# Optimization experiments

Hardware: AMD Instinct MI355X
Metric: run time of the kernel (lower is better)

The kernel has to match this reference:

```python
import jax, jax.numpy as jnp
import numpy as np

B, S, V, D, H, L, C = 64, 128, 50000, 300, 128, 20, 3
EPS = 1e-8


def lstm(x, w_ih, w_hh, b):
    # x: (B,S,D) -> outputs (B,S,H); torch gate order i,f,g,o
    xg = jnp.einsum('bsd,gd->bsg', x, w_ih) + b  # (B,S,4H)
    Hh = w_hh.shape[1]

    def step(carry, xt):
        hprev, cprev = carry
        g = xt + hprev @ w_hh.T
        i, f, gg, o = jnp.split(g, 4, axis=-1)
        c = jax.nn.sigmoid(f) * cprev + jax.nn.sigmoid(i) * jnp.tanh(gg)
        hnew = jax.nn.sigmoid(o) * jnp.tanh(c)
        return (hnew, c), hnew

    z = jnp.zeros((x.shape[0], Hh), x.dtype)
    _, hs = jax.lax.scan(step, (z, z), xg.transpose(1, 0, 2))
    return hs.transpose(1, 0, 2)


def bilstm(x, wih_f, whh_f, b_f, wih_b, whh_b, b_b):
    fwd = lstm(x, wih_f, whh_f, b_f)
    bwd = jnp.flip(lstm(jnp.flip(x, 1), wih_b, whh_b, b_b), 1)
    return jnp.concatenate([fwd, bwd], axis=-1)


def safe_div(prod, norm):
    # matches module's cosine_similarity eps handling
    return prod / jnp.where(norm > EPS, norm, EPS)


def full_matching(p1, p2, w):
    # p1: (B,S,H), p2: (B,H), w: (H,L) -> (B,S,L)
    v1 = p1[:, :, :, None] * w          # (B,S,H,L)
    v2 = p2[:, :, None] * w             # (B,H,L)
    dot = jnp.einsum('bshl,bhl->bsl', v1, v2)
    n1 = jnp.linalg.norm(v1, axis=2)    # (B,S,L)
    n2 = jnp.linalg.norm(v2, axis=1)    # (B,L)
    return dot / (jnp.maximum(n1, EPS) * jnp.maximum(n2, EPS)[:, None, :])


def maxpool_matching(p1, p2, w):
    v1 = p1[..., None] * w              # (B,S,H,L)
    v2 = p2[..., None] * w              # (B,T,H,L)
    prod = jnp.einsum('bshl,bthl->blst', v1, v2)
    n1 = jnp.linalg.norm(v1, axis=2)    # (B,S,L)
    n2 = jnp.linalg.norm(v2, axis=2)    # (B,T,L)
    deno = jnp.einsum('bsl,btl->blst', n1, n2)
    return safe_div(prod, deno).max(axis=3).transpose(0, 2, 1)  # (B,S,L)


def _wcos(a, b, w):
    # F.cosine_similarity over hidden dim of a*w vs b*w -> (B,S,L)
    va = a[..., None] * w
    vb = b[..., None] * w
    dot = jnp.einsum('bshl,bshl->bsl', va, vb)
    na = jnp.linalg.norm(va, axis=2)
    nb = jnp.linalg.norm(vb, axis=2)
    return dot / (jnp.maximum(na, EPS) * jnp.maximum(nb, EPS))


def attentive_matching(p1, p2, w_att, w_max):
    n1 = jnp.linalg.norm(p1, axis=2, keepdims=True)   # (B,S,1)
    n2 = jnp.linalg.norm(p2, axis=2, keepdims=True)   # (B,T,1)
    alpha = safe_div(jnp.einsum('bsh,bth->bst', p1, p2),
                     n1 * n2.transpose(0, 2, 1))       # (B,S,T)
    max_idx = jnp.argmax(alpha, axis=2)                # (B,S)
    h_mat = jnp.einsum('bst,bth->bsh', alpha, p2)
    resultant = h_mat / alpha.sum(axis=2, keepdims=True)
    result_match = _wcos(resultant, p1, w_att)
    out_mat = jnp.take_along_axis(p2, max_idx[..., None], axis=1)  # (B,S,H)
    result_max = _wcos(out_mat, p1, w_max)
    return result_match, result_max


def setup_inputs() -> dict:
    key = jax.random.key(0)
    ks = jax.random.split(key, 32)
    g = lambda k, shp, s=0.05: (jax.random.normal(k, shp, jnp.float32) * s)
    inp = {
        'emb': g(ks[0], (V, D), 0.1),
        'ctx_wih_f': g(ks[1], (4 * H, D)), 'ctx_whh_f': g(ks[2], (4 * H, H)), 'ctx_b_f': jnp.zeros((4 * H,), jnp.float32),
        'ctx_wih_b': g(ks[3], (4 * H, D)), 'ctx_whh_b': g(ks[4], (4 * H, H)), 'ctx_b_b': jnp.zeros((4 * H,), jnp.float32),
        'agg_wih_f': g(ks[5], (4 * H, 8 * L)), 'agg_whh_f': g(ks[6], (4 * H, H)), 'agg_b_f': jnp.zeros((4 * H,), jnp.float32),
        'agg_wih_b': g(ks[7], (4 * H, 8 * L)), 'agg_whh_b': g(ks[8], (4 * H, H)), 'agg_b_b': jnp.zeros((4 * H,), jnp.float32),
        'pW1': g(ks[9], (2 * H, 4 * H)), 'pb1': jnp.zeros((2 * H,), jnp.float32),
        'pW2': g(ks[10], (C, 2 * H)), 'pb2': jnp.zeros((C,), jnp.float32),
        'p': jax.random.randint(ks[11], (B, S), 0, V),
        'h': jax.random.randint(ks[12], (B, S), 0, V),
    }
    for i in range(1, 9):
        inp[f'w{i}'] = g(ks[12 + i], (H, L), 0.5)
    return inp


def reference(emb, ctx_wih_f, ctx_whh_f, ctx_b_f, ctx_wih_b, ctx_whh_b, ctx_b_b,
              agg_wih_f, agg_whh_f, agg_b_f, agg_wih_b, agg_whh_b, agg_b_b,
              pW1, pb1, pW2, pb2, w1, w2, w3, w4, w5, w6, w7, w8, p, h):
    p1_in = emb[p]
    p2_in = emb[h]
    c1 = bilstm(p1_in, ctx_wih_f, ctx_whh_f, ctx_b_f, ctx_wih_b, ctx_whh_b, ctx_b_b)
    c2 = bilstm(p2_in, ctx_wih_f, ctx_whh_f, ctx_b_f, ctx_wih_b, ctx_whh_b, ctx_b_b)
    c1f, c1b = jnp.split(c1, 2, axis=-1)
    c2f, c2b = jnp.split(c2, 2, axis=-1)

    match_p1_f = full_matching(c1f, c2f[:, -1], w1)
    match_p1_b = full_matching(c1b, c2b[:, -1], w2)
    match_p2_f = full_matching(c2f, c1f[:, -1], w1)
    match_p2_b = full_matching(c2b, c1b[:, -1], w2)

    maxm_p1_f = maxpool_matching(c1f, c2f, w3)
    maxm_p1_b = maxpool_matching(c1b, c2b, w4)
    maxm_p2_f = maxpool_matching(c2f, c1f, w3)
    maxm_p2_b = maxpool_matching(c2b, c1b, w4)

    att_p1_f, attm_p1_f = attentive_matching(c1f, c2f, w5, w7)
    att_p1_b, attm_p1_b = attentive_matching(c1b, c2b, w6, w8)
    att_p2_f, attm_p2_f = attentive_matching(c2f, c1f, w5, w7)
    att_p2_b, attm_p2_b = attentive_matching(c2b, c1b, w6, w8)

    aggr_p1 = jnp.concatenate([match_p1_f, match_p1_b, maxm_p1_f, maxm_p1_b,
                               att_p1_f, att_p1_b, attm_p1_f, attm_p1_b], axis=2)
    aggr_p2 = jnp.concatenate([match_p2_f, match_p2_b, maxm_p2_f, maxm_p2_b,
                               att_p2_f, att_p2_b, attm_p2_f, attm_p2_b], axis=2)

    agg_p = bilstm(aggr_p1, agg_wih_f, agg_whh_f, agg_b_f, agg_wih_b, agg_whh_b, agg_b_b)
    agg_h = bilstm(aggr_p2, agg_wih_f, agg_whh_f, agg_b_f, agg_wih_b, agg_whh_b, agg_b_b)
    out = jnp.concatenate([agg_p[:, -1], agg_h[:, -1]], axis=1)  # (B,4H)
    out = jax.nn.relu(out @ pW1.T + pb1) @ pW2.T + pb2
    return out
```

## Files before the change

kernel.cpp:

```cpp
#include <hip/hip_runtime.h>
#include <math.h>

#define B_  64
#define S_  128
#define H_  128
#define D_  300
#define L_  20
#define G4  512
#define SH  (S_*H_)
#define BSH ((size_t)B_*SH)
#define EPSV 1e-8f

typedef __attribute__((ext_vector_type(8))) short bshort8;
typedef __attribute__((ext_vector_type(4))) float f32x4;

__device__ __forceinline__ unsigned fmap(float f){
  unsigned u = __float_as_uint(f);
  return (u & 0x80000000u) ? ~u : (u | 0x80000000u);
}
__device__ __forceinline__ float funmap(unsigned u){
  return __uint_as_float((u & 0x80000000u) ? (u & 0x7fffffffu) : ~u);
}
__device__ __forceinline__ float sigmf(float x){ return 1.f/(1.f+expf(-x)); }
__device__ __forceinline__ float dot4(float4 a, float4 b){
  return a.x*b.x + a.y*b.y + a.z*b.z + a.w*b.w;
}
__device__ __forceinline__ float blane(float v, int k){
  return __int_as_float(__builtin_amdgcn_readlane(__float_as_int(v), k));
}
__device__ __forceinline__ unsigned short f2bf(float f){
  unsigned u = __float_as_uint(f);
  unsigned r = u + 0x7fffu + ((u >> 16) & 1u);
  return (unsigned short)(r >> 16);
}
__device__ __forceinline__ float bf2f(unsigned short us){
  return __uint_as_float(((unsigned)us) << 16);
}
__device__ __forceinline__ int swz64(int row, int h){
  return (row << 6) + ((((h >> 2) ^ ((row >> 3) & 15)) << 2) | (h & 3));
}
__device__ __forceinline__ int swz128(int row, int h){
  return (row << 7) + ((((h >> 2) ^ ((row >> 3) & 15)) << 2) | (h & 3));
}
__device__ __forceinline__ int bswz(int row, int slot){
  return (row << 7) + (((slot ^ (row & 15)) << 3));
}
__device__ __forceinline__ void cvt8(float4 a0, float4 a1, int4& hi, int4& lo){
  float v[8] = {a0.x, a0.y, a0.z, a0.w, a1.x, a1.y, a1.z, a1.w};
  unsigned short h[8], l[8];
  #pragma unroll
  for (int i = 0; i < 8; i++) {
    h[i] = f2bf(v[i]);
    float d = v[i] - bf2f(h[i]);
    l[i] = f2bf(d);
  }
  hi = make_int4((unsigned)h[0] | ((unsigned)h[1] << 16), (unsigned)h[2] | ((unsigned)h[3] << 16),
                 (unsigned)h[4] | ((unsigned)h[5] << 16), (unsigned)h[6] | ((unsigned)h[7] << 16));
  lo = make_int4((unsigned)l[0] | ((unsigned)l[1] << 16), (unsigned)l[2] | ((unsigned)l[3] << 16),
                 (unsigned)l[4] | ((unsigned)l[5] << 16), (unsigned)l[6] | ((unsigned)l[7] << 16));
}

__global__ void k_embed(const float* __restrict__ emb, const int* __restrict__ p,
                        const int* __restrict__ h, float* __restrict__ x1,
                        float* __restrict__ x2)
{
  int row = blockIdx.x;
  const int* idx = blockIdx.y ? h : p;
  float* x = blockIdx.y ? x2 : x1;
  int tok = idx[row];
  const float* src = emb + (size_t)tok * D_;
  float* dst = x + (size_t)row * D_;
  for (int d = threadIdx.x; d < D_; d += blockDim.x) dst[d] = src[d];
}

template<int K>
__global__ __launch_bounds__(512, 1) void gemm_abt(
    const float* __restrict__ A0, const float* __restrict__ A1,
    const float* __restrict__ W0, const float* __restrict__ W1,
    const float* __restrict__ b0, const float* __restrict__ b1,
    float* __restrict__ Cbase, int M, int N)
{
  int q = blockIdx.z;
  const float* A = (q >> 1) ? A1 : A0;
  const float* W = (q & 1) ? W1 : W0;
  const float* bias = (q & 1) ? b1 : b0;
  float* Cm = Cbase + (size_t)q * M * N;

  __shared__ __align__(16) short AsH[128 * 32];
  __shared__ __align__(16) short AsL[128 * 32];
  __shared__ __align__(16) short WsH[128 * 32];
  __shared__ __align__(16) short WsL[128 * 32];

  int t = threadIdx.x;
  int w = t >> 6, lane = t & 63;
  int r = lane & 15, g = lane >> 4;
  int m0 = blockIdx.x * 128, n0 = blockIdx.y * 128;
  int mbase = (w & 1) * 64;
  int nbase = (w >> 1) * 32;

  f32x4 acc[4][2];
  #pragma unroll
  for (int i = 0; i < 4; i++)
    #pragma unroll
    for (int j = 0; j < 2; j++) acc[i][j] = (f32x4){0.f, 0.f, 0.f, 0.f};

  int srow = t >> 2, skc = t & 3;
  int soff = srow * 32 + ((skc ^ ((srow >> 1) & 3)) << 3);

  #pragma unroll 1
  for (int k0 = 0; k0 < K; k0 += 32) {
    {
      int gk = k0 + (skc << 3);
      float4 z = make_float4(0.f, 0.f, 0.f, 0.f);
      float4 a0v = z, a1v = z, w0v = z, w1v = z;
      if (gk < K) {
        a0v = *(const float4*)&A[(size_t)(m0 + srow) * K + gk];
        w0v = *(const float4*)&W[(size_t)(n0 + srow) * K + gk];
      }
      if (gk + 4 < K) {
        a1v = *(const float4*)&A[(size_t)(m0 + srow) * K + gk + 4];
        w1v = *(const float4*)&W[(size_t)(n0 + srow) * K + gk + 4];
      }
      int4 hi, lo;
      cvt8(a0v, a1v, hi, lo);
      *(int4*)&AsH[soff] = hi; *(int4*)&AsL[soff] = lo;
      cvt8(w0v, w1v, hi, lo);
      *(int4*)&WsH[soff] = hi; *(int4*)&WsL[soff] = lo;
    }
    __syncthreads();
    bshort8 ah[4], al[4], bh[2], bl[2];
    #pragma unroll
    for (int i = 0; i < 4; i++) {
      int R = mbase + i * 16 + r;
      int off = R * 32 + ((g ^ ((R >> 1) & 3)) << 3);
      ah[i] = *(const bshort8*)&AsH[off];
      al[i] = *(const bshort8*)&AsL[off];
    }
    #pragma unroll
    for (int j = 0; j < 2; j++) {
      int R = nbase + j * 16 + r;
      int off = R * 32 + ((g ^ ((R >> 1) & 3)) << 3);
      bh[j] = *(const bshort8*)&WsH[off];
      bl[j] = *(const bshort8*)&WsL[off];
    }
    #pragma unroll
    for (int i = 0; i < 4; i++)
      #pragma unroll
      for (int j = 0; j < 2; j++) {
        acc[i][j] = __builtin_amdgcn_mfma_f32_16x16x32_bf16(ah[i], bh[j], acc[i][j], 0, 0, 0);
        acc[i][j] = __builtin_amdgcn_mfma_f32_16x16x32_bf16(ah[i], bl[j], acc[i][j], 0, 0, 0);
        acc[i][j] = __builtin_amdgcn_mfma_f32_16x16x32_bf16(al[i], bh[j], acc[i][j], 0, 0, 0);
      }
    __syncthreads();
  }
  #pragma unroll
  for (int j = 0; j < 2; j++) {
    int gcol = n0 + nbase + j * 16 + r;
    float bv = bias[gcol];
    #pragma unroll
    for (int i = 0; i < 4; i++) {
      #pragma unroll
      for (int rg = 0; rg < 4; rg++) {
        int grow = m0 + mbase + i * 16 + g * 4 + rg;
        Cm[(size_t)grow * N + gcol] = acc[i][j][rg] + bv;
      }
    }
  }
}

__global__ __launch_bounds__(1024, 1) void k_lstm(const float* __restrict__ xg,
    const float* __restrict__ whhF, const float* __restrict__ whhB,
    float* __restrict__ hs)
{
  int b = blockIdx.x, q = blockIdx.y, dir = q & 1;
  const float* whh = dir ? whhB : whhF;
  const float* xgq = xg + ((size_t)(q * B_ + b)) * (S_ * G4);
  float* out = hs + ((size_t)(q * B_ + b)) * SH;
  int tid = threadIdx.x;
  int j = tid & 511, half = tid >> 9;
  int lane = tid & 63;

  float w[64];
  {
    const float* wrow = whh + (size_t)j * 128 + half * 64;
    #pragma unroll
    for (int k = 0; k < 64; k += 4) {
      float4 v = *(const float4*)(wrow + k);
      w[k] = v.x; w[k + 1] = v.y; w[k + 2] = v.z; w[k + 3] = v.w;
    }
  }
  __shared__ float hsm[128];
  __shared__ float csm[128];
  __shared__ float gsm[2][512];
  if (tid < 128) { hsm[tid] = 0.f; csm[tid] = 0.f; }
  __syncthreads();

  float hreg = 0.f;
  float xnext = (half == 0) ? xgq[(size_t)(dir ? (S_ - 1) : 0) * G4 + j] : 0.f;

  for (int st = 0; st < S_; st++) {
    int tt = dir ? (S_ - 1 - st) : st;
    float xcur = xnext;
    if (half == 0) {
      int stn = (st + 1 < S_) ? st + 1 : st;
      int ttn = dir ? (S_ - 1 - stn) : stn;
      xnext = xgq[(size_t)ttn * G4 + j];
    }
    float a0 = xcur, a1 = 0.f, a2 = 0.f, a3 = 0.f;
    #pragma unroll
    for (int k = 0; k < 64; k += 4) {
      a0 += w[k]     * blane(hreg, k);
      a1 += w[k + 1] * blane(hreg, k + 1);
      a2 += w[k + 2] * blane(hreg, k + 2);
      a3 += w[k + 3] * blane(hreg, k + 3);
    }
    gsm[half][j] = (a0 + a1) + (a2 + a3);
    __syncthreads();
    if (tid < 128) {
      float gi = gsm[0][tid]       + gsm[1][tid];
      float gf = gsm[0][128 + tid] + gsm[1][128 + tid];
      float gg = gsm[0][256 + tid] + gsm[1][256 + tid];
      float go = gsm[0][384 + tid] + gsm[1][384 + tid];
      float ig = sigmf(gi);
      float fg = sigmf(gf);
      float gv = tanhf(gg);
      float og = sigmf(go);
      float c = fg * csm[tid] + ig * gv;
      float hn = og * tanhf(c);
      csm[tid] = c; hsm[tid] = hn;
      out[(size_t)tt * H_ + tid] = hn;
    }
    __syncthreads();
    hreg = hsm[half * 64 + lane];
  }
}

__global__ __launch_bounds__(256) void k_full(const float* __restrict__ C,
    const float* __restrict__ w1, const float* __restrict__ w2,
    float* __restrict__ ag1, float* __restrict__ ag2)
{
  int b = blockIdx.x, q = blockIdx.y, dir = q & 1;
  const float* p1  = C + (size_t)q * BSH + (size_t)b * SH;
  const float* p2l = C + (size_t)((q + 2) & 3) * BSH + (size_t)b * SH + (size_t)(S_ - 1) * H_;
  const float* w = dir ? w2 : w1;
  float* out = (q < 2 ? ag1 : ag2) + (size_t)b * S_ * 160;

  __shared__ float p1s[SH];
  __shared__ float ws2[H_][L_];
  __shared__ float p2s[H_];
  __shared__ float n2s[L_];
  int t = threadIdx.x;
  for (int i = t; i < SH; i += 256) p1s[i] = p1[i];
  for (int i = t; i < H_ * L_; i += 256) { float v = w[i]; ws2[i / L_][i % L_] = v * v; }
  if (t < H_) p2s[t] = p2l[t];
  __syncthreads();
  if (t < L_) {
    float s = 0.f;
    for (int hh = 0; hh < H_; hh++) { float v = p2s[hh]; s += v * v * ws2[hh][t]; }
    n2s[t] = sqrtf(s);
  }
  __syncthreads();
  for (int i = t; i < S_ * L_; i += 256) {
    int s = i / L_, l = i % L_;
    const float* pr = p1s + s * H_;
    float dot = 0.f, n1 = 0.f;
    for (int hh = 0; hh < H_; hh++) {
      float a = pr[hh], ww = ws2[hh][l];
      dot += a * p2s[hh] * ww;
      n1 += a * a * ww;
    }
    n1 = sqrtf(n1);
    out[(size_t)s * 160 + dir * L_ + l] = dot / (fmaxf(n1, EPSV) * fmaxf(n2s[l], EPSV));
  }
}

__global__ __launch_bounds__(512, 1) void k_maxpool(const float* __restrict__ C,
    const float* __restrict__ w3, const float* __restrict__ w4,
    float* __restrict__ ag1, float* __restrict__ ag2)
{
  int b = blockIdx.x, dir = blockIdx.y, lh = blockIdx.z;
  const float* p1 = C + (size_t)(0 + dir) * BSH + (size_t)b * SH;
  const float* p2 = C + (size_t)(2 + dir) * BSH + (size_t)b * SH;
  const float* w = dir ? w4 : w3;

  __shared__ __align__(16) short P1b[128 * 128];
  __shared__ __align__(16) short P2b[128 * 128];
  __shared__ __align__(16) short Ab[128 * 128];
  __shared__ float w2s[128 * 10];
  __shared__ float n1s[128], n2s[128];
  __shared__ unsigned mx2u[128];

  int t = threadIdx.x;
  int wv = t >> 6, lane = t & 63;
  int g = lane >> 4, col = lane & 15;

  for (int i = t; i < 8192; i += 512) {
    int row = i >> 6, hp = i & 63;
    int phys = bswz(row, hp >> 2) + ((hp & 3) << 1);
    float2 v1 = *(const float2*)&p1[(row << 7) + (hp << 1)];
    float2 v2 = *(const float2*)&p2[(row << 7) + (hp << 1)];
    *(unsigned*)&P1b[phys] = (unsigned)f2bf(v1.x) | ((unsigned)f2bf(v1.y) << 16);
    *(unsigned*)&P2b[phys] = (unsigned)f2bf(v2.x) | ((unsigned)f2bf(v2.y) << 16);
  }
  for (int i = t; i < 128 * 10; i += 512) {
    int hh = i / 10, lq = i % 10;
    float wv_ = w[hh * L_ + lh * 10 + lq];
    w2s[i] = wv_ * wv_;
  }
  __syncthreads();

  #pragma unroll 1
  for (int lq = 0; lq < 10; lq++) {
    int lout = lh * 10 + lq;
    for (int i = t; i < 8192; i += 512) {
      int row = i >> 6, hp = i & 63;
      int phys = bswz(row, hp >> 2) + ((hp & 3) << 1);
      unsigned u = *(const unsigned*)&P1b[phys];
      float lo = bf2f((unsigned short)(u & 0xffffu)) * w2s[(hp << 1) * 10 + lq];
      float hi = bf2f((unsigned short)(u >> 16))     * w2s[((hp << 1) + 1) * 10 + lq];
      *(unsigned*)&Ab[phys] = (unsigned)f2bf(lo) | ((unsigned)f2bf(hi) << 16);
    }
    {
      int s = t >> 2, part = t & 3;
      float s1 = 0.f, s2 = 0.f;
      #pragma unroll 1
      for (int hp = part * 16; hp < part * 16 + 16; hp++) {
        int phys = bswz(s, hp >> 2) + ((hp & 3) << 1);
        unsigned u1 = *(const unsigned*)&P1b[phys];
        unsigned u2 = *(const unsigned*)&P2b[phys];
        float wlo = w2s[(hp << 1) * 10 + lq];
        float whi = w2s[((hp << 1) + 1) * 10 + lq];
        float a = bf2f((unsigned short)(u1 & 0xffffu)), bb = bf2f((unsigned short)(u1 >> 16));
        float c2 = bf2f((unsigned short)(u2 & 0xffffu)), d2 = bf2f((unsigned short)(u2 >> 16));
        s1 += a * a * wlo + bb * bb * whi;
        s2 += c2 * c2 * wlo + d2 * d2 * whi;
      }
      s1 += __shfl_xor(s1, 1, 64); s1 += __shfl_xor(s1, 2, 64);
      s2 += __shfl_xor(s2, 1, 64); s2 += __shfl_xor(s2, 2, 64);
      if (part == 0) { n1s[s] = sqrtf(s1); n2s[s] = sqrtf(s2); }
    }
    if (t < 128) mx2u[t] = fmap(-3.4e38f);
    __syncthreads();

    {
      int mrow = (wv << 4) + col;
      f32x4 acc0 = {0,0,0,0}, acc1 = {0,0,0,0}, acc2 = {0,0,0,0}, acc3 = {0,0,0,0};
      f32x4 acc4 = {0,0,0,0}, acc5 = {0,0,0,0}, acc6 = {0,0,0,0}, acc7 = {0,0,0,0};
      #pragma unroll 1
      for (int k0 = 0; k0 < 128; k0 += 32) {
        int slot = ((k0 >> 3) + g) ^ col;
        bshort8 av = *(const bshort8*)&Ab[(mrow << 7) + (slot << 3)];
        bshort8 bv0 = *(const bshort8*)&P2b[((0 << 4) + col << 7) + (slot << 3)];
        bshort8 bv1 = *(const bshort8*)&P2b[(((1 << 4) + col) << 7) + (slot << 3)];
        bshort8 bv2 = *(const bshort8*)&P2b[(((2 << 4) + col) << 7) + (slot << 3)];
        bshort8 bv3 = *(const bshort8*)&P2b[(((3 << 4) + col) << 7) + (slot << 3)];
        bshort8 bv4 = *(const bshort8*)&P2b[(((4 << 4) + col) << 7) + (slot << 3)];
        bshort8 bv5 = *(const bshort8*)&P2b[(((5 << 4) + col) << 7) + (slot << 3)];
        bshort8 bv6 = *(const bshort8*)&P2b[(((6 << 4) + col) << 7) + (slot << 3)];
        bshort8 bv7 = *(const bshort8*)&P2b[(((7 << 4) + col) << 7) + (slot << 3)];
        acc0 = __builtin_amdgcn_mfma_f32_16x16x32_bf16(av, bv0, acc0, 0, 0, 0);
        acc1 = __builtin_amdgcn_mfma_f32_16x16x32_bf16(av, bv1, acc1, 0, 0, 0);
        acc2 = __builtin_amdgcn_mfma_f32_16x16x32_bf16(av, bv2, acc2, 0, 0, 0);
        acc3 = __builtin_amdgcn_mfma_f32_16x16x32_bf16(av, bv3, acc3, 0, 0, 0);
        acc4 = __builtin_amdgcn_mfma_f32_16x16x32_bf16(av, bv4, acc4, 0, 0, 0);
        acc5 = __builtin_amdgcn_mfma_f32_16x16x32_bf16(av, bv5, acc5, 0, 0, 0);
        acc6 = __builtin_amdgcn_mfma_f32_16x16x32_bf16(av, bv6, acc6, 0, 0, 0);
        acc7 = __builtin_amdgcn_mfma_f32_16x16x32_bf16(av, bv7, acc7, 0, 0, 0);
      }
      float n1v[4];
      #pragma unroll
      for (int r = 0; r < 4; r++) n1v[r] = n1s[(wv << 4) + (g << 2) + r];
      float rm[4] = {-3.4e38f, -3.4e38f, -3.4e38f, -3.4e38f};
      float cm[8];
      f32x4 accs[8] = {acc0, acc1, acc2, acc3, acc4, acc5, acc6, acc7};
      #pragma unroll
      for (int c = 0; c < 8; c++) {
        float n2v = n2s[(c << 4) + col];
        float cmx = -3.4e38f;
        #pragma unroll
        for (int r = 0; r < 4; r++) {
          float deno = n1v[r] * n2v;
          float cs = accs[c][r] / (deno > EPSV ? deno : EPSV);
          rm[r] = fmaxf(rm[r], cs);
          cmx = fmaxf(cmx, cs);
        }
        cm[c] = cmx;
      }
      #pragma unroll
      for (int m = 1; m < 16; m <<= 1)
        #pragma unroll
        for (int r = 0; r < 4; r++) rm[r] = fmaxf(rm[r], __shfl_xor(rm[r], m, 64));
      if (col == 0) {
        #pragma unroll
        for (int r = 0; r < 4; r++) {
          int srow = (wv << 4) + (g << 2) + r;
          ag1[(size_t)b * S_ * 160 + (size_t)srow * 160 + 40 + dir * L_ + lout] = rm[r];
        }
      }
      #pragma unroll
      for (int c = 0; c < 8; c++) {
        cm[c] = fmaxf(cm[c], __shfl_xor(cm[c], 16, 64));
        cm[c] = fmaxf(cm[c], __shfl_xor(cm[c], 32, 64));
      }
      if (lane < 16) {
        #pragma unroll
        for (int c = 0; c < 8; c++) atomicMax(&mx2u[(c << 4) + lane], fmap(cm[c]));
      }
    }
    __syncthreads();
    if (t < 128)
      ag2[(size_t)b * S_ * 160 + (size_t)t * 160 + 40 + dir * L_ + lout] = funmap(mx2u[t]);
    __syncthreads();
  }
}

__global__ __launch_bounds__(256, 1) void k_alpha(const float* __restrict__ C,
                                                  float* __restrict__ alpha)
{
  int b = blockIdx.x, dir = blockIdx.y;
  const float* p1 = C + (size_t)(0 + dir) * BSH + (size_t)b * SH;
  const float* p2 = C + (size_t)(2 + dir) * BSH + (size_t)b * SH;
  __shared__ __align__(16) float a1[128 * 64];
  __shared__ __align__(16) float a2[128 * 64];
  __shared__ float n1p[128], n2p[128];
  int t = threadIdx.x, tx = t & 15, ty = t >> 4;
  float acc[8][8] = {};

  for (int pass = 0; pass < 2; pass++) {
    int h0 = pass << 6;
    for (int i = t; i < 128 * 64; i += 256) {
      int row = i >> 6, hh = i & 63;
      int off = swz64(row, hh);
      a1[off] = p1[(size_t)row * H_ + h0 + hh];
      a2[off] = p2[(size_t)row * H_ + h0 + hh];
    }
    __syncthreads();
    {
      int r = t & 127;
      const float* a = (t < 128) ? a1 : a2;
      float s = 0.f;
      #pragma unroll 1
      for (int f = 0; f < 16; f++) {
        float4 v = *(const float4*)&a[(r << 6) + ((f ^ ((r >> 3) & 15)) << 2)];
        s += dot4(v, v);
      }
      float* np = (t < 128) ? n1p : n2p;
      if (pass == 0) np[r] = s; else np[r] += s;
    }
    #pragma unroll 1
    for (int f = 0; f < 16; f++) {
      int cx = ((f ^ ty) << 2);
      int cy = ((f ^ tx) << 2);
      float4 x[8], y[8];
      #pragma unroll
      for (int i = 0; i < 8; i++) x[i] = *(const float4*)&a1[((8 * ty + i) << 6) + cx];
      #pragma unroll
      for (int j = 0; j < 8; j++) y[j] = *(const float4*)&a2[((8 * tx + j) << 6) + cy];
      #pragma unroll
      for (int i = 0; i < 8; i++)
        #pragma unroll
        for (int j = 0; j < 8; j++) acc[i][j] += dot4(x[i], y[j]);
    }
    __syncthreads();
  }
  float inv1[8], inv2[8];
  #pragma unroll
  for (int i = 0; i < 8; i++) inv1[i] = 1.f / fmaxf(sqrtf(n1p[8 * ty + i]), EPSV);
  #pragma unroll
  for (int j = 0; j < 8; j++) inv2[j] = 1.f / fmaxf(sqrtf(n2p[8 * tx + j]), EPSV);
  float* outp = alpha + ((size_t)dir * B_ + b) * SH;
  #pragma unroll
  for (int i = 0; i < 8; i++) {
    int ss = 8 * ty + i;
    float s1 = inv1[i];
    float4 o0 = make_float4(acc[i][0] * s1 * inv2[0], acc[i][1] * s1 * inv2[1],
                            acc[i][2] * s1 * inv2[2], acc[i][3] * s1 * inv2[3]);
    float4 o1 = make_float4(acc[i][4] * s1 * inv2[4], acc[i][5] * s1 * inv2[5],
                            acc[i][6] * s1 * inv2[6], acc[i][7] * s1 * inv2[7]);
    *(float4*)&outp[(size_t)ss * S_ + 8 * tx] = o0;
    *(float4*)&outp[(size_t)ss * S_ + 8 * tx + 4] = o1;
  }
}

__global__ __launch_bounds__(256, 1) void k_att(const float* __restrict__ C,
    const float* __restrict__ alpha,
    const float* __restrict__ w5, const float* __restrict__ w6,
    const float* __restrict__ w7, const float* __restrict__ w8,
    float* __restrict__ ag1, float* __restrict__ ag2)
{
  int b = blockIdx.x, q = blockIdx.y, dir = q & 1;
  const float* p1  = C + (size_t)q * BSH + (size_t)b * SH;
  const float* m2g = C + (size_t)((q + 2) & 3) * BSH + (size_t)b * SH;
  const float* wa = dir ? w6 : w5;
  const float* wm = dir ? w8 : w7;
  const float* ain = alpha + ((size_t)dir * B_ + b) * SH;
  float* out = (q < 2 ? ag1 : ag2) + (size_t)b * S_ * 160;
  bool tr = (q >= 2);

  __shared__ __align__(16) float A[128 * 128];
  __shared__ __align__(16) float M2T[128 * 128];
  __shared__ __align__(16) float waT[20 * 128];
  __shared__ __align__(16) float wmT[20 * 128];
  __shared__ float rowsum[128];
  __shared__ int   midx[128];
  int t = threadIdx.x, tx = t & 15, ty = t >> 4;

  for (int i = t; i < SH; i += 256) {
    int r = i >> 7, c = i & 127;
    float av = ain[i];
    if (tr) A[swz128(c, r)] = av; else A[swz128(r, c)] = av;
    M2T[swz128(c, r)] = m2g[i];
  }
  for (int i = t; i < H_ * L_; i += 256) {
    int hh = i / L_, l = i % L_;
    float v = wa[i]; waT[l * 128 + hh] = v * v;
    float u = wm[i]; wmT[l * 128 + hh] = u * u;
  }
  __syncthreads();

  if (t < 128) {
    float sum = 0.f, best = -3.4e38f; int bi = 0;
    #pragma unroll 1
    for (int f = 0; f < 32; f++) {
      float4 v = *(const float4*)&A[(t << 7) + (((f ^ ((t >> 3) & 15)) & 31) << 2)];
      sum += v.x + v.y + v.z + v.w;
      int k = f << 2;
      if (v.x > best) { best = v.x; bi = k; }
      if (v.y > best) { best = v.y; bi = k + 1; }
      if (v.z > best) { best = v.z; bi = k + 2; }
      if (v.w > best) { best = v.w; bi = k + 3; }
    }
    rowsum[t] = sum; midx[t] = bi;
  }
  __syncthreads();

  float acc[8][8] = {};
  #pragma unroll 1
  for (int f = 0; f < 32; f++) {
    int cx = (((f ^ ty) & 31) << 2);
    int cy = (((f ^ tx) & 31) << 2);
    float4 x[8], y[8];
    #pragma unroll
    for (int i = 0; i < 8; i++) x[i] = *(const float4*)&A[((8 * ty + i) << 7) + cx];
    #pragma unroll
    for (int j = 0; j < 8; j++) y[j] = *(const float4*)&M2T[((8 * tx + j) << 7) + cy];
    #pragma unroll
    for (int i = 0; i < 8; i++)
      #pragma unroll
      for (int j = 0; j < 8; j++) acc[i][j] += dot4(x[i], y[j]);
  }
  __syncthreads();
  {
    float rinv[8];
    #pragma unroll
    for (int i = 0; i < 8; i++) rinv[i] = 1.f / rowsum[8 * ty + i];
    #pragma unroll
    for (int i = 0; i < 8; i++) {
      int row = 8 * ty + i;
      int f0 = (2 * tx) ^ ((row >> 3) & 15);
      int f1 = (2 * tx + 1) ^ ((row >> 3) & 15);
      float4 o0 = make_float4(acc[i][0] * rinv[i], acc[i][1] * rinv[i],
                              acc[i][2] * rinv[i], acc[i][3] * rinv[i]);
      float4 o1 = make_float4(acc[i][4] * rinv[i], acc[i][5] * rinv[i],
                              acc[i][6] * rinv[i], acc[i][7] * rinv[i]);
      *(float4*)&A[(row << 7) + (f0 << 2)] = o0;
      *(float4*)&A[(row << 7) + (f1 << 2)] = o1;
    }
  }
  __syncthreads();

  {
    int s = t >> 1, l0 = (t & 1) * 10;
    int mi = midx[s];
    const float* m2r = m2g + (size_t)mi * H_;
    const float* p1r = p1 + (size_t)s * H_;
    float dA[10] = {}, nA[10] = {}, bA[10] = {};
    float dM[10] = {}, nM[10] = {}, bM[10] = {};
    #pragma unroll 1
    for (int f = 0; f < 32; f++) {
      float4 pv = *(const float4*)&p1r[f << 2];
      float4 mv = *(const float4*)&m2r[f << 2];
      float4 av = *(const float4*)&A[(s << 7) + (((f ^ ((s >> 3) & 15)) & 31) << 2)];
      float4 ap = make_float4(av.x*pv.x, av.y*pv.y, av.z*pv.z, av.w*pv.w);
      float4 a2 = make_float4(av.x*av.x, av.y*av.y, av.z*av.z, av.w*av.w);
      float4 p2 = make_float4(pv.x*pv.x, pv.y*pv.y, pv.z*pv.z, pv.w*pv.w);
      float4 mp = make_float4(mv.x*pv.x, mv.y*pv.y, mv.z*pv.z, mv.w*pv.w);
      float4 m2 = make_float4(mv.x*mv.x, mv.y*mv.y, mv.z*mv.z, mv.w*mv.w);
      #pragma unroll
      for (int l = 0; l < 10; l++) {
        float4 wv = *(const float4*)&waT[(l0 + l) * 128 + (f << 2)];
        dA[l] += dot4(ap, wv); nA[l] += dot4(a2, wv); bA[l] += dot4(p2, wv);
        float4 uv = *(const float4*)&wmT[(l0 + l) * 128 + (f << 2)];
        dM[l] += dot4(mp, uv); nM[l] += dot4(m2, uv); bM[l] += dot4(p2, uv);
      }
    }
    #pragma unroll
    for (int l = 0; l < 10; l++) {
      int ll = l0 + l;
      out[(size_t)s * 160 + 80  + dir * L_ + ll] =
          dA[l] / (fmaxf(sqrtf(nA[l]), EPSV) * fmaxf(sqrtf(bA[l]), EPSV));
      out[(size_t)s * 160 + 120 + dir * L_ + ll] =
          dM[l] / (fmaxf(sqrtf(nM[l]), EPSV) * fmaxf(sqrtf(bM[l]), EPSV));
    }
  }
}

__global__ __launch_bounds__(256) void k_final(const float* __restrict__ Cc,
    const float* __restrict__ pW1, const float* __restrict__ pb1,
    const float* __restrict__ pW2, const float* __restrict__ pb2,
    float* __restrict__ out)
{
  int b = blockIdx.x, t = threadIdx.x;
  __shared__ float cat[512];
  __shared__ float hid[256];
  if (t < 128) {
    cat[t]       = Cc[(size_t)(0 * B_ + b) * SH + (size_t)(S_ - 1) * H_ + t];
    cat[128 + t] = Cc[(size_t)(1 * B_ + b) * SH + (size_t)(S_ - 1) * H_ + t];
    cat[256 + t] = Cc[(size_t)(2 * B_ + b) * SH + (size_t)(S_ - 1) * H_ + t];
    cat[384 + t] = Cc[(size_t)(3 * B_ + b) * SH + (size_t)(S_ - 1) * H_ + t];
  }
  __syncthreads();
  float a = pb1[t];
  for (int k = 0; k < 512; k++) a += cat[k] * pW1[(size_t)t * 512 + k];
  hid[t] = fmaxf(a, 0.f);
  __syncthreads();
  if (t < 3) {
    float o = pb2[t];
    for (int k = 0; k < 256; k++) o += hid[k] * pW2[(size_t)t * 256 + k];
    out[(size_t)b * 3 + t] = o;
  }
}

extern "C" void kernel_launch(void* const* d_in, const int* in_sizes, int n_in,
                              void* d_out, int out_size, void* d_ws, size_t ws_size,
                              hipStream_t stream)
{
  const float* emb    = (const float*)d_in[0];
  const float* cwih_f = (const float*)d_in[1];
  const float* cwhh_f = (const float*)d_in[2];
  const float* cb_f   = (const float*)d_in[3];
  const float* cwih_b = (const float*)d_in[4];
  const float* cwhh_b = (const float*)d_in[5];
  const float* cb_b   = (const float*)d_in[6];
  const float* awih_f = (const float*)d_in[7];
  const float* awhh_f = (const float*)d_in[8];
  const float* ab_f   = (const float*)d_in[9];
  const float* awih_b = (const float*)d_in[10];
  const float* awhh_b = (const float*)d_in[11];
  const float* ab_b   = (const float*)d_in[12];
  const float* pW1    = (const float*)d_in[13];
  const float* pb1    = (const float*)d_in[14];
  const float* pW2    = (const float*)d_in[15];
  const float* pb2    = (const float*)d_in[16];
  const int*   pidx   = (const int*)d_in[17];
  const int*   hidx   = (const int*)d_in[18];
  const float* w1 = (const float*)d_in[19];
  const float* w2 = (const float*)d_in[20];
  const float* w3 = (const float*)d_in[21];
  const float* w4 = (const float*)d_in[22];
  const float* w5 = (const float*)d_in[23];
  const float* w6 = (const float*)d_in[24];
  const float* w7 = (const float*)d_in[25];
  const float* w8 = (const float*)d_in[26];

  float* ws = (float*)d_ws;
  float* XG   = ws;
  float* X1   = ws + 16777216;
  float* X2   = X1 + 2457600;
  float* ALPH = X1;
  float* AG1  = ws + 16777216 + 2097152;
  float* AG2  = AG1 + (size_t)B_ * S_ * 160;
  float* CC   = ws + 21692416;

  k_embed<<<dim3(B_ * S_, 2), 256, 0, stream>>>(emb, pidx, hidx, X1, X2);
  gemm_abt<D_><<<dim3(64, 4, 4), 512, 0, stream>>>(X1, X2, cwih_f, cwih_b, cb_f, cb_b,
                                                   XG, B_ * S_, G4);
  k_lstm<<<dim3(B_, 4), 1024, 0, stream>>>(XG, cwhh_f, cwhh_b, CC);
  k_full<<<dim3(B_, 4), 256, 0, stream>>>(CC, w1, w2, AG1, AG2);
  k_maxpool<<<dim3(B_, 2, 2), 512, 0, stream>>>(CC, w3, w4, AG1, AG2);
  k_alpha<<<dim3(B_, 2), 256, 0, stream>>>(CC, ALPH);
  k_att<<<dim3(B_, 4), 256, 0, stream>>>(CC, ALPH, w5, w6, w7, w8, AG1, AG2);
  gemm_abt<8 * L_><<<dim3(64, 4, 4), 512, 0, stream>>>(AG1, AG2, awih_f, awih_b, ab_f, ab_b,
                                                       XG, B_ * S_, G4);
  k_lstm<<<dim3(B_, 4), 1024, 0, stream>>>(XG, awhh_f, awhh_b, CC);
  k_final<<<dim3(B_), 256, 0, stream>>>(CC, pW1, pb1, pW2, pb2, (float*)d_out);
}
```

Before: 658.9 us.

## Halve LSTM block size and replace second barrier with redundant per-wave gate update

The recurrent LSTM kernel now runs 512 threads instead of 1024. Each thread computes two gate rows, keeping 128 recurrent weights in registers as float2 pairs. Gate partial sums go into a double-buffered shared array indexed by step parity. Every wave then recomputes the cell and hidden update redundantly for its own 64 hidden slots, so the second __syncthreads per step and the shared h/c arrays are gone. This cuts per-step barrier latency on the serial 128-step chain, at the cost of doubled register pressure and duplicated transcendental work across waves.

```diff
diff --git a/kernel.cpp b/kernel.cpp
--- a/kernel.cpp
+++ b/kernel.cpp
@@ -168,7 +168,7 @@
   }
 }
 
-__global__ __launch_bounds__(1024, 1) void k_lstm(const float* __restrict__ xg,
+__global__ __launch_bounds__(512, 1) void k_lstm(const float* __restrict__ xg,
     const float* __restrict__ whhF, const float* __restrict__ whhB,
     float* __restrict__ hs)
 {
@@ -176,62 +176,75 @@
   const float* whh = dir ? whhB : whhF;
   const float* xgq = xg + ((size_t)(q * B_ + b)) * (S_ * G4);
   float* out = hs + ((size_t)(q * B_ + b)) * SH;
-  int tid = threadIdx.x;
-  int j = tid & 511, half = tid >> 9;
-  int lane = tid & 63;
-
-  float w[64];
+  int t = threadIdx.x;
+  int j = t & 255;
+  int kh = t >> 8;
+  int lane = t & 63;
+  int wvid = t >> 6;
+  int hidx = kh * 64 + lane;
+
+  float2 w2[64];
   {
-    const float* wrow = whh + (size_t)j * 128 + half * 64;
+    const float* wr0 = whh + (size_t)j * 128 + kh * 64;
+    const float* wr1 = whh + (size_t)(j + 256) * 128 + kh * 64;
     #pragma unroll
     for (int k = 0; k < 64; k += 4) {
-      float4 v = *(const float4*)(wrow + k);
-      w[k] = v.x; w[k + 1] = v.y; w[k + 2] = v.z; w[k + 3] = v.w;
-    }
-  }
-  __shared__ float hsm[128];
-  __shared__ float csm[128];
-  __shared__ float gsm[2][512];
-  if (tid < 128) { hsm[tid] = 0.f; csm[tid] = 0.f; }
-  __syncthreads();
-
-  float hreg = 0.f;
-  float xnext = (half == 0) ? xgq[(size_t)(dir ? (S_ - 1) : 0) * G4 + j] : 0.f;
+      float4 v0 = *(const float4*)(wr0 + k);
+      float4 v1 = *(const float4*)(wr1 + k);
+      w2[k]     = make_float2(v0.x, v1.x);
+      w2[k + 1] = make_float2(v0.y, v1.y);
+      w2[k + 2] = make_float2(v0.z, v1.z);
+      w2[k + 3] = make_float2(v0.w, v1.w);
+    }
+  }
+  __shared__ float gsm[2][2][512];
+
+  float creg = 0.f, hreg = 0.f;
+  float xn0 = 0.f, xn1 = 0.f;
+  if (kh == 0) {
+    int t0 = dir ? (S_ - 1) : 0;
+    xn0 = xgq[(size_t)t0 * G4 + j];
+    xn1 = xgq[(size_t)t0 * G4 + j + 256];
+  }
 
   for (int st = 0; st < S_; st++) {
     int tt = dir ? (S_ - 1 - st) : st;
-    float xcur = xnext;
-    if (half == 0) {
+    float x0 = xn0, x1 = xn1;
+    if (kh == 0) {
       int stn = (st + 1 < S_) ? st + 1 : st;
       int ttn = dir ? (S_ - 1 - stn) : stn;
-      xnext = xgq[(size_t)ttn * G4 + j];
-    }
-    float a0 = xcur, a1 = 0.f, a2 = 0.f, a3 = 0.f;
+      xn0 = xgq[(size_t)ttn * G4 + j];
+      xn1 = xgq[(size_t)ttn * G4 + j + 256];
+    }
+    float a0x = (kh == 0) ? x0 : 0.f, a0y = (kh == 0) ? x1 : 0.f;
+    float a1x = 0.f, a1y = 0.f, a2x = 0.f, a2y = 0.f, a3x = 0.f, a3y = 0.f;
     #pragma unroll
     for (int k = 0; k < 64; k += 4) {
-      a0 += w[k]     * blane(hreg, k);
-      a1 += w[k + 1] * blane(hreg, k + 1);
-      a2 += w[k + 2] * blane(hreg, k + 2);
-      a3 += w[k + 3] * blane(hreg, k + 3);
-    }
-    gsm[half][j] = (a0 + a1) + (a2 + a3);
+      float s0 = blane(hreg, k);
+      float s1 = blane(hreg, k + 1);
+      float s2 = blane(hreg, k + 2);
+      float s3 = blane(hreg, k + 3);
+      a0x += w2[k].x * s0;     a0y += w2[k].y * s0;
+      a1x += w2[k + 1].x * s1; a1y += w2[k + 1].y * s1;
+      a2x += w2[k + 2].x * s2; a2y += w2[k + 2].y * s2;
+      a3x += w2[k + 3].x * s3; a3y += w2[k + 3].y * s3;
+    }
+    int par = st & 1;
+    gsm[par][kh][j]       = (a0x + a1x) + (a2x + a3x);
+    gsm[par][kh][j + 256] = (a0y + a1y) + (a2y + a3y);
     __syncthreads();
-    if (tid < 128) {
-      float gi = gsm[0][tid]       + gsm[1][tid];
-      float gf = gsm[0][128 + tid] + gsm[1][128 + tid];
-      float gg = gsm[0][256 + tid] + gsm[1][256 + tid];
-      float go = gsm[0][384 + tid] + gsm[1][384 + tid];
-      float ig = sigmf(gi);
-      float fg = sigmf(gf);
-      float gv = tanhf(gg);
-      float og = sigmf(go);
-      float c = fg * csm[tid] + ig * gv;
-      float hn = og * tanhf(c);
-      csm[tid] = c; hsm[tid] = hn;
-      out[(size_t)tt * H_ + tid] = hn;
-    }
-    __syncthreads();
-    hreg = hsm[half * 64 + lane];
+    float gi = gsm[par][0][hidx]       + gsm[par][1][hidx];
+    float gf = gsm[par][0][128 + hidx] + gsm[par][1][128 + hidx];
+    float gg = gsm[par][0][256 + hidx] + gsm[par][1][256 + hidx];
+    float go = gsm[par][0][384 + hidx] + gsm[par][1][384 + hidx];
+    float ig = sigmf(gi);
+    float fg = sigmf(gf);
+    float gv = tanhf(gg);
+    float og = sigmf(go);
+    creg = fg * creg + ig * gv;
+    hreg = og * tanhf(creg);
+    if (wvid == 0 || wvid == 4)
+      out[(size_t)tt * H_ + hidx] = hreg;
   }
 }
 
@@ -675,13 +688,13 @@
   k_embed<<<dim3(B_ * S_, 2), 256, 0, stream>>>(emb, pidx, hidx, X1, X2);
   gemm_abt<D_><<<dim3(64, 4, 4), 512, 0, stream>>>(X1, X2, cwih_f, cwih_b, cb_f, cb_b,
                                                    XG, B_ * S_, G4);
-  k_lstm<<<dim3(B_, 4), 1024, 0, stream>>>(XG, cwhh_f, cwhh_b, CC);
+  k_lstm<<<dim3(B_, 4), 512, 0, stream>>>(XG, cwhh_f, cwhh_b, CC);
   k_full<<<dim3(B_, 4), 256, 0, stream>>>(CC, w1, w2, AG1, AG2);
   k_maxpool<<<dim3(B_, 2, 2), 512, 0, stream>>>(CC, w3, w4, AG1, AG2);
   k_alpha<<<dim3(B_, 2), 256, 0, stream>>>(CC, ALPH);
   k_att<<<dim3(B_, 4), 256, 0, stream>>>(CC, ALPH, w5, w6, w7, w8, AG1, AG2);
   gemm_abt<8 * L_><<<dim3(64, 4, 4), 512, 0, stream>>>(AG1, AG2, awih_f, awih_b, ab_f, ab_b,
                                                        XG, B_ * S_, G4);
-  k_lstm<<<dim3(B_, 4), 1024, 0, stream>>>(XG, awhh_f, awhh_b, CC);
+  k_lstm<<<dim3(B_, 4), 512, 0, stream>>>(XG, awhh_f, awhh_b, CC);
   k_final<<<dim3(B_), 256, 0, stream>>>(CC, pW1, pb1, pW2, pb2, (float*)d_out);
 }
```

Measured after the change: 668.6 us. Within noise of the previous version (+1.5%).
